# Kernel tuning notes

Hardware: AMD Instinct MI355X
Metric: run time of the kernel (lower is better)

## Reference

```python
import jax, jax.numpy as jnp
import numpy as np

N, E, B, DIM = 50000, 800000, 64, 64

def setup_inputs() -> dict:
    key = jax.random.key(0)
    ks = jax.random.split(key, 8)
    x = jax.random.normal(ks[0], (N, DIM), dtype=jnp.float32)
    edge_index = jax.random.randint(ks[1], (2, E), 0, N, dtype=jnp.int64)
    edge_attr = jax.random.normal(ks[2], (E, DIM), dtype=jnp.float32)
    u = jax.random.normal(ks[3], (B, DIM), dtype=jnp.float32)
    batch = jnp.sort(jax.random.randint(ks[4], (N,), 0, B, dtype=jnp.int64))
    # MLP params: Linear(3*dim, dim) -> ReLU -> Linear(dim, dim)
    s1 = 1.0 / np.sqrt(3 * DIM)
    s2 = 1.0 / np.sqrt(DIM)
    W1 = jax.random.uniform(ks[5], (3 * DIM, DIM), minval=-s1, maxval=s1, dtype=jnp.float32)
    b1 = jnp.zeros((DIM,), dtype=jnp.float32)
    W2 = jax.random.uniform(ks[6], (DIM, DIM), minval=-s2, maxval=s2, dtype=jnp.float32)
    b2 = jnp.zeros((DIM,), dtype=jnp.float32)
    return {"x": x, "edge_index": edge_index, "edge_attr": edge_attr, "u": u,
            "batch": batch, "W1": W1, "b1": b1, "W2": W2, "b2": b2}

def reference(x, edge_index, edge_attr, u, batch, W1, b1, W2, b2):
    src = edge_index[0]
    # scatter_mean(edge_attr, src, dim=0) -> [N, DIM]; empty segments give 0
    sums = jax.ops.segment_sum(edge_attr, src, num_segments=N)
    counts = jax.ops.segment_sum(jnp.ones((E,), dtype=edge_attr.dtype), src, num_segments=N)
    v_e = sums / jnp.maximum(counts, 1.0)[:, None]
    comb = jnp.concatenate([x, v_e, u[batch]], axis=1)  # [N, 3*DIM]
    h = jax.nn.relu(comb @ W1 + b1)
    return h @ W2 + b2
```

## Files before the change

kernel.cpp:

```cpp
#include <hip/hip_runtime.h>

#define NN 50000
#define NE 800000
#define NB 64
#define DIM 64
#define TM 128
#define CAP 64
#define EB 4096
#define NBLK_A 196
#define NBKT 392
#define BN 128

typedef float vfloat4 __attribute__((ext_vector_type(4)));


__global__ __launch_bounds__(1024) void bucketA_k(const int* __restrict__ src,
                                                  int* __restrict__ bbuf,
                                                  int* __restrict__ blkoff,
                                                  const float* __restrict__ u,
                                                  const float* __restrict__ W1,
                                                  const float* __restrict__ b1,
                                                  float* __restrict__ U1) {
    __shared__ int hist[NBKT];
    __shared__ int cnt2[NBKT];
    __shared__ int off[NBKT + 1];
    __shared__ int sortedE[EB];

    const int tid = threadIdx.x;
    const int blk = blockIdx.x;

    for (int i = tid; i < NBKT; i += 1024) { hist[i] = 0; cnt2[i] = 0; }
    __syncthreads();

    const int e0 = (blk * 1024 + tid) * 4;
    const bool valid = (e0 < NE);
    int4 s4 = make_int4(0, 0, 0, 0);
    if (valid) s4 = ((const int4*)src)[e0 >> 2];
    const int bk0 = s4.x >> 7, bk1 = s4.y >> 7, bk2 = s4.z >> 7, bk3 = s4.w >> 7;

    if (valid) {
        atomicAdd(&hist[bk0], 1);
        atomicAdd(&hist[bk1], 1);
        atomicAdd(&hist[bk2], 1);
        atomicAdd(&hist[bk3], 1);
    }
    __syncthreads();

    if (tid < 64) {
        const int base = tid * 8;
        int a[8];
        int sum = 0;
        #pragma unroll
        for (int i = 0; i < 8; ++i) {
            a[i] = (base + i < NBKT) ? hist[base + i] : 0;
            sum += a[i];
        }
        int run = sum;
        #pragma unroll
        for (int m = 1; m < 64; m <<= 1) {
            int v = __shfl_up(run, m, 64);
            if (tid >= m) run += v;
        }
        int acc2 = run - sum;
        #pragma unroll
        for (int i = 0; i < 8; ++i) {
            if (base + i < NBKT) off[base + i] = acc2;
            acc2 += a[i];
        }
        if (tid == 63) off[NBKT] = run;
    }
    __syncthreads();

    if (valid) {
        int r0 = off[bk0] + atomicAdd(&cnt2[bk0], 1); sortedE[r0] = e0 + 0;
        int r1 = off[bk1] + atomicAdd(&cnt2[bk1], 1); sortedE[r1] = e0 + 1;
        int r2 = off[bk2] + atomicAdd(&cnt2[bk2], 1); sortedE[r2] = e0 + 2;
        int r3 = off[bk3] + atomicAdd(&cnt2[bk3], 1); sortedE[r3] = e0 + 3;
    }
    __syncthreads();

    const int nE = min(EB, NE - blk * EB);
    for (int i = tid; i < nE; i += 1024)
        bbuf[blk * EB + i] = sortedE[i];
    for (int i = tid; i <= NBKT; i += 1024)
        blkoff[blk * (NBKT + 1) + i] = off[i];

    if (blk < NB && tid < DIM) {
        float a = b1[tid];
        const float* up = u + blk * DIM;
        #pragma unroll 8
        for (int k = 0; k < DIM; ++k)
            a = fmaf(up[k], W1[(2 * DIM + k) * DIM + tid], a);
        U1[blk * DIM + tid] = a;
    }
}

__global__ __launch_bounds__(1024) void placeRed_k(const int* __restrict__ src,
                                                   const int* __restrict__ bbuf,
                                                   const int* __restrict__ blkoff,
                                                   const vfloat4* __restrict__ ea4,
                                                   float4* __restrict__ ve4) {
    __shared__ int eids_l[BN * CAP];
    __shared__ int cnt[BN];
    __shared__ int lo_s[NBLK_A], hi_s[NBLK_A];
    __shared__ int segoff[NBLK_A + 1];

    const int b = blockIdx.x;
    const int tid = threadIdx.x;

    if (tid < BN) cnt[tid] = 0;
    if (tid < NBLK_A) {
        lo_s[tid] = blkoff[tid * (NBKT + 1) + b];
        hi_s[tid] = blkoff[tid * (NBKT + 1) + b + 1];
    }
    __syncthreads();

    if (tid < 64) {
        const int base = tid * 4;
        int a0 = 0, a1 = 0, a2 = 0, a3 = 0;
        if (base < NBLK_A) {
            a0 = hi_s[base + 0] - lo_s[base + 0];
            a1 = hi_s[base + 1] - lo_s[base + 1];
            a2 = hi_s[base + 2] - lo_s[base + 2];
            a3 = hi_s[base + 3] - lo_s[base + 3];
        }
        const int sum = a0 + a1 + a2 + a3;
        int run = sum;
        #pragma unroll
        for (int m = 1; m < 64; m <<= 1) {
            int v = __shfl_up(run, m, 64);
            if (tid >= m) run += v;
        }
        const int excl = run - sum;
        if (base < NBLK_A) {
            segoff[base + 0] = excl;
            segoff[base + 1] = excl + a0;
            segoff[base + 2] = excl + a0 + a1;
            segoff[base + 3] = excl + a0 + a1 + a2;
        }
        if (tid == 63) segoff[NBLK_A] = run;
    }
    __syncthreads();

    const int total = segoff[NBLK_A];
    for (int i = tid; i < total; i += 1024) {
        int lo2 = 0, hi2 = NBLK_A;
        while (lo2 + 1 < hi2) {
            int mid = (lo2 + hi2) >> 1;
            if (segoff[mid] <= i) lo2 = mid; else hi2 = mid;
        }
        const int blk = lo2;
        const int idx = i - segoff[blk] + lo_s[blk];
        const int e = bbuf[blk * EB + idx];
        const int s = src[e];
        const int nl = s & (BN - 1);
        const int rank = atomicAdd(&cnt[nl], 1);
        if (rank < CAP) eids_l[nl * CAP + rank] = e;
    }
    __syncthreads();

    const int wave = tid >> 6, lane = tid & 63;
    const int chunk = lane & 15, slot = lane >> 4;
    const vfloat4 vzero = {0.f, 0.f, 0.f, 0.f};

    #pragma unroll
    for (int m = 0; m < BN / 16; ++m) {
        const int nl = wave * (BN / 16) + m;
        const int n = b * BN + nl;
        if (n >= NN) break;
        const int deg = min(cnt[nl], CAP);
        const int* ebase = eids_l + nl * CAP;

        vfloat4 acc = vzero;
        if (deg > 0) {
            const int dm1 = deg - 1;
            int e[8];
            #pragma unroll
            for (int r = 0; r < 8; ++r) {
                int j = slot + r * 4;
                e[r] = ebase[j < dm1 ? j : dm1];
            }
            #pragma unroll
            for (int r = 0; r < 8; ++r) {
                vfloat4 v = __builtin_nontemporal_load(&ea4[(size_t)e[r] * 16 + chunk]);
                acc += (slot + r * 4 < deg) ? v : vzero;
            }
            for (int j = 32 + slot; j < deg; j += 4) {
                int ee = ebase[j];
                vfloat4 v = __builtin_nontemporal_load(&ea4[(size_t)ee * 16 + chunk]);
                acc += v;
            }
        }
        #pragma unroll
        for (int mm = 16; mm <= 32; mm <<= 1) {
            acc.x += __shfl_xor(acc.x, mm, 64);
            acc.y += __shfl_xor(acc.y, mm, 64);
            acc.z += __shfl_xor(acc.z, mm, 64);
            acc.w += __shfl_xor(acc.w, mm, 64);
        }
        if (slot == 0) {
            const float rs = 1.0f / fmaxf((float)cnt[nl], 1.0f);
            ve4[(size_t)n * 16 + chunk] =
                make_float4(acc.x * rs, acc.y * rs, acc.z * rs, acc.w * rs);
        }
    }
}

#define LDA 132

__device__ __forceinline__ void gemm4(float acc[4][4],
                                      const float* __restrict__ A,
                                      const float* __restrict__ Wb,
                                      int NG, int DG) {
    #pragma unroll 4
    for (int k = 0; k < 64; ++k) {
        const float4 w = *(const float4*)&Wb[k * 64 + DG];
        const float4 a = *(const float4*)&A[k * LDA + NG];
        const float av[4] = {a.x, a.y, a.z, a.w};
        const float wv[4] = {w.x, w.y, w.z, w.w};
        #pragma unroll
        for (int i = 0; i < 4; ++i)
            #pragma unroll
            for (int j = 0; j < 4; ++j)
                acc[i][j] = fmaf(av[i], wv[j], acc[i][j]);
    }
}

__global__ __launch_bounds__(512) void mlp_k(const float* __restrict__ x,
                                             const int* __restrict__ batch,
                                             const float* __restrict__ W1,
                                             const float* __restrict__ W2,
                                             const float* __restrict__ b2,
                                             const float* __restrict__ ve,
                                             const float* __restrict__ U1,
                                             float* __restrict__ out) {
    __shared__ float A[64 * LDA];
    __shared__ float Wb[64 * 64];

    const int t = threadIdx.x;
    const int c = t & 15;
    const int rb = t >> 4;
    const int DG = (t & 15) * 4;
    const int NG = (t >> 4) * 4;
    const int n0 = blockIdx.x * TM;

    float acc[4][4];

    #pragma unroll
    for (int i = 0; i < 4; ++i) {
        int n = n0 + NG + i;
        int b = (n < NN) ? batch[n] : 0;
        const float4 uv = *(const float4*)&U1[b * DIM + DG];
        acc[i][0] = uv.x; acc[i][1] = uv.y; acc[i][2] = uv.z; acc[i][3] = uv.w;
    }

    #pragma unroll
    for (int it = 0; it < 4; ++it) {
        int r = rb + it * 32;
        int n = n0 + r;
        float4 v = make_float4(0.f, 0.f, 0.f, 0.f);
        if (n < NN) v = *(const float4*)&x[(size_t)n * DIM + c * 4];
        A[(c * 4 + 0) * LDA + r] = v.x;
        A[(c * 4 + 1) * LDA + r] = v.y;
        A[(c * 4 + 2) * LDA + r] = v.z;
        A[(c * 4 + 3) * LDA + r] = v.w;
    }
    #pragma unroll
    for (int it = 0; it < 2; ++it) {
        int r = rb + it * 32;
        *(float4*)&Wb[r * 64 + c * 4] = *(const float4*)&W1[(size_t)r * DIM + c * 4];
    }
    __syncthreads();
    gemm4(acc, A, Wb, NG, DG);
    __syncthreads();

    #pragma unroll
    for (int it = 0; it < 4; ++it) {
        int r = rb + it * 32;
        int n = n0 + r;
        float4 v = make_float4(0.f, 0.f, 0.f, 0.f);
        if (n < NN) v = *(const float4*)&ve[(size_t)n * DIM + c * 4];
        A[(c * 4 + 0) * LDA + r] = v.x;
        A[(c * 4 + 1) * LDA + r] = v.y;
        A[(c * 4 + 2) * LDA + r] = v.z;
        A[(c * 4 + 3) * LDA + r] = v.w;
    }
    #pragma unroll
    for (int it = 0; it < 2; ++it) {
        int r = rb + it * 32;
        *(float4*)&Wb[r * 64 + c * 4] = *(const float4*)&W1[(size_t)(64 + r) * DIM + c * 4];
    }
    __syncthreads();
    gemm4(acc, A, Wb, NG, DG);

    #pragma unroll
    for (int i = 0; i < 4; ++i)
        #pragma unroll
        for (int j = 0; j < 4; ++j)
            acc[i][j] = fmaxf(acc[i][j], 0.f);

    __syncthreads();

    #pragma unroll
    for (int j = 0; j < 4; ++j) {
        float4 h = make_float4(acc[0][j], acc[1][j], acc[2][j], acc[3][j]);
        *(float4*)&A[(DG + j) * LDA + NG] = h;
    }
    #pragma unroll
    for (int it = 0; it < 2; ++it) {
        int r = rb + it * 32;
        *(float4*)&Wb[r * 64 + c * 4] = *(const float4*)&W2[(size_t)r * DIM + c * 4];
    }
    __syncthreads();

    {
        const float4 bv = *(const float4*)&b2[DG];
        #pragma unroll
        for (int i = 0; i < 4; ++i) {
            acc[i][0] = bv.x; acc[i][1] = bv.y; acc[i][2] = bv.z; acc[i][3] = bv.w;
        }
    }
    gemm4(acc, A, Wb, NG, DG);

    #pragma unroll
    for (int i = 0; i < 4; ++i) {
        int n = n0 + NG + i;
        if (n < NN) {
            float4 o = make_float4(acc[i][0], acc[i][1], acc[i][2], acc[i][3]);
            *(float4*)&out[(size_t)n * DIM + DG] = o;
        }
    }
}

extern "C" void kernel_launch(void* const* d_in, const int* in_sizes, int n_in,
                              void* d_out, int out_size, void* d_ws, size_t ws_size,
                              hipStream_t stream)
{
    const float* x     = (const float*)d_in[0];
    const int*   eidx  = (const int*)d_in[1];
    const float* ea    = (const float*)d_in[2];
    const float* u     = (const float*)d_in[3];
    const int*   batch = (const int*)d_in[4];
    const float* W1    = (const float*)d_in[5];
    const float* b1    = (const float*)d_in[6];
    const float* W2    = (const float*)d_in[7];
    const float* b2    = (const float*)d_in[8];
    float* out = (float*)d_out;

    float* ve     = (float*)d_ws;
    float* U1     = ve + (size_t)NN * DIM;
    int*   bbuf   = (int*)(U1 + NB * DIM);
    int*   blkoff = bbuf + (size_t)NBLK_A * EB;

    bucketA_k<<<NBLK_A, 1024, 0, stream>>>(eidx, bbuf, blkoff, u, W1, b1, U1);
    placeRed_k<<<NBKT, 1024, 0, stream>>>(eidx, bbuf, blkoff, (const vfloat4*)ea, (float4*)ve);
    mlp_k<<<(NN + TM - 1) / TM, 512, 0, stream>>>(x, batch, W1, W2, b2, ve, U1, out);
}
```

Before: 89.47 us.

## Fuse edge mean reduction into MLP kernel and pack local node id in bucket entries

The per-node mean aggregation of edge features now runs in the same kernel as the MLP. The means are written straight into the shared-memory A tile instead of round-tripping through a global ve buffer, which removes a full N×64 float write and read plus one kernel launch. The bucketing kernel also packs the source node's low 7 bits into the upper bits of each edge id, so the placement phase no longer has to gather src[e]. In exchange the fused kernel runs with 512 threads instead of 1024, leaving fewer waves to hide gather latency. It also holds more shared memory per block, and the mean now divides by the capped degree rather than the full count.

After: 76.32 us, median of 2. -14.7%, faster.

```diff
diff --git a/kernel.cpp b/kernel.cpp
--- a/kernel.cpp
+++ b/kernel.cpp
@@ -4,12 +4,12 @@
 #define NE 800000
 #define NB 64
 #define DIM 64
-#define TM 128
 #define CAP 64
 #define EB 4096
 #define NBLK_A 196
 #define NBKT 392
 #define BN 128
+#define LDA 132
 
 typedef float vfloat4 __attribute__((ext_vector_type(4)));
 
@@ -72,10 +72,10 @@
     __syncthreads();
 
     if (valid) {
-        int r0 = off[bk0] + atomicAdd(&cnt2[bk0], 1); sortedE[r0] = e0 + 0;
-        int r1 = off[bk1] + atomicAdd(&cnt2[bk1], 1); sortedE[r1] = e0 + 1;
-        int r2 = off[bk2] + atomicAdd(&cnt2[bk2], 1); sortedE[r2] = e0 + 2;
-        int r3 = off[bk3] + atomicAdd(&cnt2[bk3], 1); sortedE[r3] = e0 + 3;
+        int r0 = off[bk0] + atomicAdd(&cnt2[bk0], 1); sortedE[r0] = (e0 + 0) | ((s4.x & 127) << 20);
+        int r1 = off[bk1] + atomicAdd(&cnt2[bk1], 1); sortedE[r1] = (e0 + 1) | ((s4.y & 127) << 20);
+        int r2 = off[bk2] + atomicAdd(&cnt2[bk2], 1); sortedE[r2] = (e0 + 2) | ((s4.z & 127) << 20);
+        int r3 = off[bk3] + atomicAdd(&cnt2[bk3], 1); sortedE[r3] = (e0 + 3) | ((s4.w & 127) << 20);
     }
     __syncthreads();
 
@@ -94,119 +94,6 @@
         U1[blk * DIM + tid] = a;
     }
 }
-
-__global__ __launch_bounds__(1024) void placeRed_k(const int* __restrict__ src,
-                                                   const int* __restrict__ bbuf,
-                                                   const int* __restrict__ blkoff,
-                                                   const vfloat4* __restrict__ ea4,
-                                                   float4* __restrict__ ve4) {
-    __shared__ int eids_l[BN * CAP];
-    __shared__ int cnt[BN];
-    __shared__ int lo_s[NBLK_A], hi_s[NBLK_A];
-    __shared__ int segoff[NBLK_A + 1];
-
-    const int b = blockIdx.x;
-    const int tid = threadIdx.x;
-
-    if (tid < BN) cnt[tid] = 0;
-    if (tid < NBLK_A) {
-        lo_s[tid] = blkoff[tid * (NBKT + 1) + b];
-        hi_s[tid] = blkoff[tid * (NBKT + 1) + b + 1];
-    }
-    __syncthreads();
-
-    if (tid < 64) {
-        const int base = tid * 4;
-        int a0 = 0, a1 = 0, a2 = 0, a3 = 0;
-        if (base < NBLK_A) {
-            a0 = hi_s[base + 0] - lo_s[base + 0];
-            a1 = hi_s[base + 1] - lo_s[base + 1];
-            a2 = hi_s[base + 2] - lo_s[base + 2];
-            a3 = hi_s[base + 3] - lo_s[base + 3];
-        }
-        const int sum = a0 + a1 + a2 + a3;
-        int run = sum;
-        #pragma unroll
-        for (int m = 1; m < 64; m <<= 1) {
-            int v = __shfl_up(run, m, 64);
-            if (tid >= m) run += v;
-        }
-        const int excl = run - sum;
-        if (base < NBLK_A) {
-            segoff[base + 0] = excl;
-            segoff[base + 1] = excl + a0;
-            segoff[base + 2] = excl + a0 + a1;
-            segoff[base + 3] = excl + a0 + a1 + a2;
-        }
-        if (tid == 63) segoff[NBLK_A] = run;
-    }
-    __syncthreads();
-
-    const int total = segoff[NBLK_A];
-    for (int i = tid; i < total; i += 1024) {
-        int lo2 = 0, hi2 = NBLK_A;
-        while (lo2 + 1 < hi2) {
-            int mid = (lo2 + hi2) >> 1;
-            if (segoff[mid] <= i) lo2 = mid; else hi2 = mid;
-        }
-        const int blk = lo2;
-        const int idx = i - segoff[blk] + lo_s[blk];
-        const int e = bbuf[blk * EB + idx];
-        const int s = src[e];
-        const int nl = s & (BN - 1);
-        const int rank = atomicAdd(&cnt[nl], 1);
-        if (rank < CAP) eids_l[nl * CAP + rank] = e;
-    }
-    __syncthreads();
-
-    const int wave = tid >> 6, lane = tid & 63;
-    const int chunk = lane & 15, slot = lane >> 4;
-    const vfloat4 vzero = {0.f, 0.f, 0.f, 0.f};
-
-    #pragma unroll
-    for (int m = 0; m < BN / 16; ++m) {
-        const int nl = wave * (BN / 16) + m;
-        const int n = b * BN + nl;
-        if (n >= NN) break;
-        const int deg = min(cnt[nl], CAP);
-        const int* ebase = eids_l + nl * CAP;
-
-        vfloat4 acc = vzero;
-        if (deg > 0) {
-            const int dm1 = deg - 1;
-            int e[8];
-            #pragma unroll
-            for (int r = 0; r < 8; ++r) {
-                int j = slot + r * 4;
-                e[r] = ebase[j < dm1 ? j : dm1];
-            }
-            #pragma unroll
-            for (int r = 0; r < 8; ++r) {
-                vfloat4 v = __builtin_nontemporal_load(&ea4[(size_t)e[r] * 16 + chunk]);
-                acc += (slot + r * 4 < deg) ? v : vzero;
-            }
-            for (int j = 32 + slot; j < deg; j += 4) {
-                int ee = ebase[j];
-                vfloat4 v = __builtin_nontemporal_load(&ea4[(size_t)ee * 16 + chunk]);
-                acc += v;
-            }
-        }
-        #pragma unroll
-        for (int mm = 16; mm <= 32; mm <<= 1) {
-            acc.x += __shfl_xor(acc.x, mm, 64);
-            acc.y += __shfl_xor(acc.y, mm, 64);
-            acc.z += __shfl_xor(acc.z, mm, 64);
-            acc.w += __shfl_xor(acc.w, mm, 64);
-        }
-        if (slot == 0) {
-            const float rs = 1.0f / fmaxf((float)cnt[nl], 1.0f);
-            ve4[(size_t)n * 16 + chunk] =
-                make_float4(acc.x * rs, acc.y * rs, acc.z * rs, acc.w * rs);
-        }
-    }
-}
-
-#define LDA 132
 
 __device__ __forceinline__ void gemm4(float acc[4][4],
                                       const float* __restrict__ A,
@@ -226,33 +113,149 @@
     }
 }
 
-__global__ __launch_bounds__(512) void mlp_k(const float* __restrict__ x,
-                                             const int* __restrict__ batch,
-                                             const float* __restrict__ W1,
-                                             const float* __restrict__ W2,
-                                             const float* __restrict__ b2,
-                                             const float* __restrict__ ve,
-                                             const float* __restrict__ U1,
-                                             float* __restrict__ out) {
+__global__ __launch_bounds__(512) void fused2_k(const int* __restrict__ bbuf,
+                                                const int* __restrict__ blkoff,
+                                                const vfloat4* __restrict__ ea4,
+                                                const float* __restrict__ x,
+                                                const int* __restrict__ batch,
+                                                const float* __restrict__ W1,
+                                                const float* __restrict__ W2,
+                                                const float* __restrict__ b2,
+                                                const float* __restrict__ U1,
+                                                float* __restrict__ out) {
+    __shared__ int eids_l[BN * CAP];
     __shared__ float A[64 * LDA];
-    __shared__ float Wb[64 * 64];
-
-    const int t = threadIdx.x;
-    const int c = t & 15;
-    const int rb = t >> 4;
-    const int DG = (t & 15) * 4;
-    const int NG = (t >> 4) * 4;
-    const int n0 = blockIdx.x * TM;
+    __shared__ int cnt[BN];
+    __shared__ int lo_s[NBLK_A], hi_s[NBLK_A];
+    __shared__ int segoff[NBLK_A + 1];
+    float* Wb = (float*)eids_l;
+
+    const int b = blockIdx.x;
+    const int tid = threadIdx.x;
+    const int n0 = b * BN;
+
+    if (tid < BN) cnt[tid] = 0;
+    for (int i = tid; i < NBLK_A; i += 512) {
+        lo_s[i] = blkoff[i * (NBKT + 1) + b];
+        hi_s[i] = blkoff[i * (NBKT + 1) + b + 1];
+    }
+    __syncthreads();
+
+    if (tid < 64) {
+        const int base = tid * 4;
+        int a0 = 0, a1 = 0, a2 = 0, a3 = 0;
+        if (base < NBLK_A) {
+            a0 = hi_s[base + 0] - lo_s[base + 0];
+            a1 = hi_s[base + 1] - lo_s[base + 1];
+            a2 = hi_s[base + 2] - lo_s[base + 2];
+            a3 = hi_s[base + 3] - lo_s[base + 3];
+        }
+        const int sum = a0 + a1 + a2 + a3;
+        int run = sum;
+        #pragma unroll
+        for (int m = 1; m < 64; m <<= 1) {
+            int v = __shfl_up(run, m, 64);
+            if (tid >= m) run += v;
+        }
+        const int excl = run - sum;
+        if (base < NBLK_A) {
+            segoff[base + 0] = excl;
+            segoff[base + 1] = excl + a0;
+            segoff[base + 2] = excl + a0 + a1;
+            segoff[base + 3] = excl + a0 + a1 + a2;
+        }
+        if (tid == 63) segoff[NBLK_A] = run;
+    }
+    __syncthreads();
+
+    const int total = segoff[NBLK_A];
+    for (int i = tid; i < total; i += 512) {
+        int lo2 = 0, hi2 = NBLK_A;
+        while (lo2 + 1 < hi2) {
+            int mid = (lo2 + hi2) >> 1;
+            if (segoff[mid] <= i) lo2 = mid; else hi2 = mid;
+        }
+        const int idx = i - segoff[lo2] + lo_s[lo2];
+        const int v = bbuf[lo2 * EB + idx];
+        const int e = v & 0xFFFFF;
+        const int nl = v >> 20;
+        const int rank = atomicAdd(&cnt[nl], 1);
+        if (rank < CAP) eids_l[nl * CAP + rank] = e;
+    }
+    __syncthreads();
+
+    {
+        const int wave = tid >> 6, lane = tid & 63;
+        const int chunk = lane & 15, slot = lane >> 4;
+        const vfloat4 vzero = {0.f, 0.f, 0.f, 0.f};
+        for (int m = 0; m < 16; ++m) {
+            const int nl = wave * 16 + m;
+            const int n = n0 + nl;
+            if (n >= NN) break;
+            const int deg = min(cnt[nl], CAP);
+            const int* ebase = eids_l + nl * CAP;
+
+            vfloat4 acc = vzero;
+            if (deg > 0) {
+                const int dm1 = deg - 1;
+                int e[8];
+                #pragma unroll
+                for (int r = 0; r < 8; ++r) {
+                    int j = slot + r * 4;
+                    e[r] = ebase[j < dm1 ? j : dm1];
+                }
+                #pragma unroll
+                for (int r = 0; r < 8; ++r) {
+                    vfloat4 v = __builtin_nontemporal_load(&ea4[(size_t)e[r] * 16 + chunk]);
+                    acc += (slot + r * 4 < deg) ? v : vzero;
+                }
+                for (int j = 32 + slot; j < deg; j += 4) {
+                    int ee = ebase[j];
+                    vfloat4 v = __builtin_nontemporal_load(&ea4[(size_t)ee * 16 + chunk]);
+                    acc += v;
+                }
+            }
+            #pragma unroll
+            for (int mm = 16; mm <= 32; mm <<= 1) {
+                acc.x += __shfl_xor(acc.x, mm, 64);
+                acc.y += __shfl_xor(acc.y, mm, 64);
+                acc.z += __shfl_xor(acc.z, mm, 64);
+                acc.w += __shfl_xor(acc.w, mm, 64);
+            }
+            if (slot == 0) {
+                const float rs = 1.0f / fmaxf((float)deg, 1.0f);
+                A[(chunk * 4 + 0) * LDA + nl] = acc.x * rs;
+                A[(chunk * 4 + 1) * LDA + nl] = acc.y * rs;
+                A[(chunk * 4 + 2) * LDA + nl] = acc.z * rs;
+                A[(chunk * 4 + 3) * LDA + nl] = acc.w * rs;
+            }
+        }
+    }
+    __syncthreads();
+
+    const int c = tid & 15;
+    const int rb = tid >> 4;
+    const int DG = c * 4;
+    const int NG = rb * 4;
 
     float acc[4][4];
 
+    #pragma unroll
+    for (int it = 0; it < 2; ++it) {
+        int r = rb + it * 32;
+        *(float4*)&Wb[r * 64 + c * 4] = *(const float4*)&W1[(size_t)(64 + r) * DIM + c * 4];
+    }
     #pragma unroll
     for (int i = 0; i < 4; ++i) {
         int n = n0 + NG + i;
-        int b = (n < NN) ? batch[n] : 0;
-        const float4 uv = *(const float4*)&U1[b * DIM + DG];
+        int bb = (n < NN) ? batch[n] : 0;
+        const float4 uv = *(const float4*)&U1[bb * DIM + DG];
         acc[i][0] = uv.x; acc[i][1] = uv.y; acc[i][2] = uv.z; acc[i][3] = uv.w;
     }
+    __syncthreads();
+
+    gemm4(acc, A, Wb, NG, DG);
+    __syncthreads();
 
     #pragma unroll
     for (int it = 0; it < 4; ++it) {
@@ -269,26 +272,6 @@
     for (int it = 0; it < 2; ++it) {
         int r = rb + it * 32;
         *(float4*)&Wb[r * 64 + c * 4] = *(const float4*)&W1[(size_t)r * DIM + c * 4];
-    }
-    __syncthreads();
-    gemm4(acc, A, Wb, NG, DG);
-    __syncthreads();
-
-    #pragma unroll
-    for (int it = 0; it < 4; ++it) {
-        int r = rb + it * 32;
-        int n = n0 + r;
-        float4 v = make_float4(0.f, 0.f, 0.f, 0.f);
-        if (n < NN) v = *(const float4*)&ve[(size_t)n * DIM + c * 4];
-        A[(c * 4 + 0) * LDA + r] = v.x;
-        A[(c * 4 + 1) * LDA + r] = v.y;
-        A[(c * 4 + 2) * LDA + r] = v.z;
-        A[(c * 4 + 3) * LDA + r] = v.w;
-    }
-    #pragma unroll
-    for (int it = 0; it < 2; ++it) {
-        int r = rb + it * 32;
-        *(float4*)&Wb[r * 64 + c * 4] = *(const float4*)&W1[(size_t)(64 + r) * DIM + c * 4];
     }
     __syncthreads();
     gemm4(acc, A, Wb, NG, DG);
@@ -347,12 +330,11 @@
     const float* b2    = (const float*)d_in[8];
     float* out = (float*)d_out;
 
-    float* ve     = (float*)d_ws;
-    float* U1     = ve + (size_t)NN * DIM;
+    float* U1     = (float*)d_ws;
     int*   bbuf   = (int*)(U1 + NB * DIM);
     int*   blkoff = bbuf + (size_t)NBLK_A * EB;
 
     bucketA_k<<<NBLK_A, 1024, 0, stream>>>(eidx, bbuf, blkoff, u, W1, b1, U1);
-    placeRed_k<<<NBKT, 1024, 0, stream>>>(eidx, bbuf, blkoff, (const vfloat4*)ea, (float4*)ve);
-    mlp_k<<<(NN + TM - 1) / TM, 512, 0, stream>>>(x, batch, W1, W2, b2, ve, U1, out);
+    fused2_k<<<NBKT, 512, 0, stream>>>(bbuf, blkoff, (const vfloat4*)ea,
+                                       x, batch, W1, W2, b2, U1, out);
 }
```
